# Kernel tuning notes

Measured on AMD Instinct MI355X. Metric: run time of the kernel, lower is better.

Reference implementation:

```python
import jax, jax.numpy as jnp
import numpy as np

D_MODEL = 1024
N_HEADS = 16
D_HEAD = D_MODEL // N_HEADS


def setup_inputs() -> dict:
    key = jax.random.key(0)
    kx, kq, kk, kv, ko = jax.random.split(key, 5)
    s = 1.0 / np.sqrt(D_MODEL)
    return {
        "x": jax.random.normal(kx, (4, 2048, D_MODEL), dtype=jnp.float32),
        "Wq": jax.random.normal(kq, (D_MODEL, D_MODEL), dtype=jnp.float32) * s,
        "Wk": jax.random.normal(kk, (D_MODEL, D_MODEL), dtype=jnp.float32) * s,
        "Wv": jax.random.normal(kv, (D_MODEL, D_MODEL), dtype=jnp.float32) * s,
        "Wo": jax.random.normal(ko, (D_MODEL, D_MODEL), dtype=jnp.float32) * s,
    }


def reference(x, Wq, Wk, Wv, Wo):
    B, L, D = x.shape
    # Projections (torch Linear: y = x @ W.T)
    q = (x @ Wq.T).reshape(B, L, N_HEADS, D_HEAD).transpose(0, 2, 1, 3)  # [B,H,L,dh]
    k = (x @ Wk.T).reshape(B, L, N_HEADS, D_HEAD).transpose(0, 2, 1, 3)
    v = (x @ Wv.T).reshape(B, L, N_HEADS, D_HEAD).transpose(0, 2, 1, 3)
    scale = 1.0 / np.sqrt(D_HEAD).astype(np.float32)
    scores = jnp.einsum('bhqd,bhkd->bhqk', q, k) * scale  # [B,H,L,L]
    causal = jnp.tril(jnp.ones((L, L), dtype=bool))
    scores = jnp.where(causal[None, None], scores, -jnp.inf)
    attn = jax.nn.softmax(scores, axis=-1)
    out = jnp.einsum('bhqk,bhkd->bhqd', attn, v)  # [B,H,L,dh]
    out = out.transpose(0, 2, 1, 3).reshape(B, L, D)
    return out @ Wo.T
```

## Files before the change

kernel.cpp:

```cpp
#include <hip/hip_runtime.h>

typedef short bf16x8 __attribute__((ext_vector_type(8)));
typedef float f32x4 __attribute__((ext_vector_type(4)));
typedef unsigned short u16;

#define MFMA16x16x32(a, b, c) __builtin_amdgcn_mfma_f32_16x16x32_bf16((a), (b), (c), 0, 0, 0)

#define BATCH 4
#define SEQ 2048
#define DMODEL 1024
#define NHEADS 16
#define DHEAD 64
#define MROWS (BATCH * SEQ)

__device__ __forceinline__ u16 f2bf(float f) {
  unsigned u = __builtin_bit_cast(unsigned, f);
  u += 0x7fffu + ((u >> 16) & 1u);
  return (u16)(u >> 16);
}

template <int CTRL>
__device__ __forceinline__ float dppmov(float x) {
  return __builtin_bit_cast(
      float, __builtin_amdgcn_mov_dpp(__builtin_bit_cast(int, x), CTRL, 0xF, 0xF, false));
}
__device__ __forceinline__ float rowmax16(float x) {
  x = fmaxf(x, dppmov<0x128>(x));
  x = fmaxf(x, dppmov<0x124>(x));
  x = fmaxf(x, dppmov<0x122>(x));
  x = fmaxf(x, dppmov<0x121>(x));
  return x;
}
__device__ __forceinline__ float rowsum16(float x) {
  x += dppmov<0x128>(x);
  x += dppmov<0x124>(x);
  x += dppmov<0x122>(x);
  x += dppmov<0x121>(x);
  return x;
}

__global__ void cvt_f32_bf16(const float* __restrict__ src, u16* __restrict__ dst, int n4) {
  int i = blockIdx.x * blockDim.x + threadIdx.x;
  if (i < n4) {
    float4 v = reinterpret_cast<const float4*>(src)[i];
    ushort4 o;
    o.x = f2bf(v.x); o.y = f2bf(v.y); o.z = f2bf(v.z); o.w = f2bf(v.w);
    reinterpret_cast<ushort4*>(dst)[i] = o;
  }
}

template <int MODE>
__global__ __launch_bounds__(256) void gemm_bt(const u16* __restrict__ A,
                                               const u16* __restrict__ Bm,
                                               void* __restrict__ dst) {
  constexpr int K = 1024;
  constexpr int LSTR = 72;
  __shared__ u16 As[128 * LSTR];
  __shared__ u16 Bs[128 * LSTR];
  const int tid = threadIdx.x;
  const int lane = tid & 63;
  const int w = tid >> 6;
  const int wr = w >> 1, wc = w & 1;
  const int quad = lane >> 4, l16 = lane & 15;
  const int row0 = blockIdx.y * 128, col0 = blockIdx.x * 128;

  f32x4 acc[4][4] = {};

  for (int k0 = 0; k0 < K; k0 += 64) {
    __syncthreads();
#pragma unroll
    for (int i = 0; i < 4; i++) {
      int ch = tid + i * 256;
      int r = ch >> 3, cg = (ch & 7) * 8;
      *reinterpret_cast<bf16x8*>(&As[r * LSTR + cg]) =
          *reinterpret_cast<const bf16x8*>(&A[(row0 + r) * K + k0 + cg]);
      *reinterpret_cast<bf16x8*>(&Bs[r * LSTR + cg]) =
          *reinterpret_cast<const bf16x8*>(&Bm[(col0 + r) * K + k0 + cg]);
    }
    __syncthreads();
#pragma unroll
    for (int ks = 0; ks < 2; ks++) {
      bf16x8 af[4], bfr[4];
#pragma unroll
      for (int i = 0; i < 4; i++)
        af[i] = *reinterpret_cast<const bf16x8*>(
            &As[(wr * 64 + i * 16 + l16) * LSTR + ks * 32 + quad * 8]);
#pragma unroll
      for (int j = 0; j < 4; j++)
        bfr[j] = *reinterpret_cast<const bf16x8*>(
            &Bs[(wc * 64 + j * 16 + l16) * LSTR + ks * 32 + quad * 8]);
#pragma unroll
      for (int i = 0; i < 4; i++)
#pragma unroll
        for (int j = 0; j < 4; j++)
          acc[i][j] = MFMA16x16x32(af[i], bfr[j], acc[i][j]);
    }
  }

#pragma unroll
  for (int i = 0; i < 4; i++)
#pragma unroll
    for (int j = 0; j < 4; j++)
#pragma unroll
      for (int r = 0; r < 4; r++) {
        int row = row0 + wr * 64 + i * 16 + quad * 4 + r;
        int col = col0 + wc * 64 + j * 16 + l16;
        float v = acc[i][j][r];
        if constexpr (MODE == 0 || MODE == 3) {
          u16* q = (u16*)dst;
          int bh = ((row >> 11) << 4) | (col >> 6);
          if constexpr (MODE == 3) v *= 0.125f;
          q[(bh * SEQ + (row & 2047)) * DHEAD + (col & 63)] = f2bf(v);
        } else if constexpr (MODE == 1) {
          u16* q = (u16*)dst;
          int bh = ((row >> 11) << 4) | (col >> 6);
          q[(bh * DHEAD + (col & 63)) * SEQ + (row & 2047)] = f2bf(v);
        } else {
          ((float*)dst)[row * DMODEL + col] = v;
        }
      }
}

__global__ __launch_bounds__(256, 3) void attn_kernel(const u16* __restrict__ Q,
                                                      const u16* __restrict__ Kk,
                                                      const u16* __restrict__ Vt,
                                                      u16* __restrict__ Ao) {
  constexpr int STR = 72;
  __shared__ u16 Ks[64 * STR];
  __shared__ u16 Vs[64 * STR];
  __shared__ u16 Plds[4][32 * STR];
  const int tid = threadIdx.x;
  const int lane = tid & 63;
  const int w = tid >> 6;
  const int quad = lane >> 4, l16 = lane & 15;
  const int bh = blockIdx.x & 63;
  const int qt = 15 - (blockIdx.x >> 6);
  const int b = bh >> 4, h = bh & 15;
  const u16* Qh = Q + bh * SEQ * DHEAD;
  const u16* Kh = Kk + bh * SEQ * DHEAD;
  const u16* Vh = Vt + bh * DHEAD * SEQ;
  const int q0w = qt * 128 + w * 32;
  const int nkt = 2 * qt + 2;

  bf16x8 qf[2][2];
#pragma unroll
  for (int rt = 0; rt < 2; rt++)
#pragma unroll
    for (int ks = 0; ks < 2; ks++)
      qf[rt][ks] = *reinterpret_cast<const bf16x8*>(
          &Qh[(q0w + rt * 16 + l16) * DHEAD + ks * 32 + quad * 8]);

  f32x4 o[2][4] = {};
  float m_i[2][4], l_i[2][4];
#pragma unroll
  for (int rt = 0; rt < 2; rt++)
#pragma unroll
    for (int r = 0; r < 4; r++) { m_i[rt][r] = -1e30f; l_i[rt][r] = 0.f; }

  const int srow = tid >> 3;
  const int scol = (tid & 7) * 8;
  bf16x8 kst[2], vst[2];
  auto load_tile = [&](int kb) {
#pragma unroll
    for (int c = 0; c < 2; c++) {
      int r = srow + c * 32;
      kst[c] = *reinterpret_cast<const bf16x8*>(&Kh[(kb + r) * DHEAD + scol]);
      vst[c] = *reinterpret_cast<const bf16x8*>(&Vh[r * SEQ + kb + scol]);
    }
  };
  auto store_tile = [&]() {
#pragma unroll
    for (int c = 0; c < 2; c++) {
      int r = srow + c * 32;
      *reinterpret_cast<bf16x8*>(&Ks[r * STR + scol]) = kst[c];
      *reinterpret_cast<bf16x8*>(&Vs[r * STR + scol]) = vst[c];
    }
  };

  load_tile(0);
  store_tile();
  __syncthreads();

  for (int kt = 0; kt < nkt; kt++) {
    const int kbase = kt * 64;
    const bool have_next = (kt + 1 < nkt);
    if (have_next) load_tile(kbase + 64);

    if (kbase <= q0w + 31) {
      f32x4 s[2][4];
#pragma unroll
      for (int nt = 0; nt < 4; nt++) {
        bf16x8 kf0 = *reinterpret_cast<const bf16x8*>(&Ks[(nt * 16 + l16) * STR + quad * 8]);
        bf16x8 kf1 = *reinterpret_cast<const bf16x8*>(&Ks[(nt * 16 + l16) * STR + 32 + quad * 8]);
#pragma unroll
        for (int rt = 0; rt < 2; rt++) {
          f32x4 z = {0.f, 0.f, 0.f, 0.f};
          z = MFMA16x16x32(qf[rt][0], kf0, z);
          s[rt][nt] = MFMA16x16x32(qf[rt][1], kf1, z);
        }
      }
      if (kbase + 63 > q0w) {
#pragma unroll
        for (int rt = 0; rt < 2; rt++)
#pragma unroll
          for (int nt = 0; nt < 4; nt++)
#pragma unroll
            for (int r = 0; r < 4; r++) {
              int qrow = q0w + rt * 16 + quad * 4 + r;
              int kcol = kbase + nt * 16 + l16;
              if (kcol > qrow) s[rt][nt][r] = -1e30f;
            }
      }
      float alpha[2][4];
#pragma unroll
      for (int rt = 0; rt < 2; rt++)
#pragma unroll
        for (int r = 0; r < 4; r++) {
          float mx = fmaxf(fmaxf(s[rt][0][r], s[rt][1][r]), fmaxf(s[rt][2][r], s[rt][3][r]));
          mx = rowmax16(mx);
          float mnew = fmaxf(m_i[rt][r], mx);
          alpha[rt][r] = __expf(m_i[rt][r] - mnew);
          m_i[rt][r] = mnew;
        }
#pragma unroll
      for (int rt = 0; rt < 2; rt++)
#pragma unroll
        for (int nt = 0; nt < 4; nt++)
#pragma unroll
          for (int r = 0; r < 4; r++)
            s[rt][nt][r] = __expf(s[rt][nt][r] - m_i[rt][r]);
#pragma unroll
      for (int rt = 0; rt < 2; rt++)
#pragma unroll
        for (int r = 0; r < 4; r++) {
          float rs = (s[rt][0][r] + s[rt][1][r]) + (s[rt][2][r] + s[rt][3][r]);
          rs = rowsum16(rs);
          l_i[rt][r] = l_i[rt][r] * alpha[rt][r] + rs;
        }
#pragma unroll
      for (int rt = 0; rt < 2; rt++)
#pragma unroll
        for (int nt = 0; nt < 4; nt++)
#pragma unroll
          for (int r = 0; r < 4; r++) o[rt][nt][r] *= alpha[rt][r];
      u16* Pw = Plds[w];
#pragma unroll
      for (int rt = 0; rt < 2; rt++)
#pragma unroll
        for (int nt = 0; nt < 4; nt++)
#pragma unroll
          for (int r = 0; r < 4; r++)
            Pw[(rt * 16 + quad * 4 + r) * STR + nt * 16 + l16] = f2bf(s[rt][nt][r]);
      asm volatile("s_waitcnt lgkmcnt(0)" ::: "memory");
      bf16x8 pa[2][2];
#pragma unroll
      for (int rt = 0; rt < 2; rt++)
#pragma unroll
        for (int hh = 0; hh < 2; hh++)
          pa[rt][hh] = *reinterpret_cast<const bf16x8*>(
              &Pw[(rt * 16 + l16) * STR + hh * 32 + quad * 8]);
#pragma unroll
      for (int nt2 = 0; nt2 < 4; nt2++) {
        bf16x8 vf0 = *reinterpret_cast<const bf16x8*>(&Vs[(nt2 * 16 + l16) * STR + quad * 8]);
        bf16x8 vf1 = *reinterpret_cast<const bf16x8*>(&Vs[(nt2 * 16 + l16) * STR + 32 + quad * 8]);
#pragma unroll
        for (int rt = 0; rt < 2; rt++) {
          o[rt][nt2] = MFMA16x16x32(pa[rt][0], vf0, o[rt][nt2]);
          o[rt][nt2] = MFMA16x16x32(pa[rt][1], vf1, o[rt][nt2]);
        }
      }
    }

    if (have_next) {
      __syncthreads();
      store_tile();
      __syncthreads();
    }
  }

#pragma unroll
  for (int rt = 0; rt < 2; rt++)
#pragma unroll
    for (int nt2 = 0; nt2 < 4; nt2++)
#pragma unroll
      for (int r = 0; r < 4; r++) {
        int qrow = q0w + rt * 16 + quad * 4 + r;
        float v = o[rt][nt2][r] / l_i[rt][r];
        Ao[(b * SEQ + qrow) * DMODEL + h * DHEAD + nt2 * 16 + l16] = f2bf(v);
      }
}

extern "C" void kernel_launch(void* const* d_in, const int* in_sizes, int n_in,
                              void* d_out, int out_size, void* d_ws, size_t ws_size,
                              hipStream_t stream) {
  const float* x = (const float*)d_in[0];
  const float* Wq = (const float*)d_in[1];
  const float* Wk = (const float*)d_in[2];
  const float* Wv = (const float*)d_in[3];
  const float* Wo = (const float*)d_in[4];
  float* out = (float*)d_out;

  u16* xb  = (u16*)d_ws;
  u16* wqb = xb  + MROWS * DMODEL;
  u16* wkb = wqb + DMODEL * DMODEL;
  u16* wvb = wkb + DMODEL * DMODEL;
  u16* wob = wvb + DMODEL * DMODEL;
  u16* qb  = wob + DMODEL * DMODEL;
  u16* kb  = qb  + MROWS * DMODEL;
  u16* vtb = kb  + MROWS * DMODEL;
  u16* aob = vtb + MROWS * DMODEL;

  {
    int n4 = MROWS * DMODEL / 4;
    cvt_f32_bf16<<<n4 / 256, 256, 0, stream>>>(x, xb, n4);
    int w4 = DMODEL * DMODEL / 4;
    cvt_f32_bf16<<<w4 / 256, 256, 0, stream>>>(Wq, wqb, w4);
    cvt_f32_bf16<<<w4 / 256, 256, 0, stream>>>(Wk, wkb, w4);
    cvt_f32_bf16<<<w4 / 256, 256, 0, stream>>>(Wv, wvb, w4);
    cvt_f32_bf16<<<w4 / 256, 256, 0, stream>>>(Wo, wob, w4);
  }

  dim3 ggrid(DMODEL / 128, MROWS / 128);
  gemm_bt<3><<<ggrid, 256, 0, stream>>>(xb, wqb, (void*)qb);
  gemm_bt<0><<<ggrid, 256, 0, stream>>>(xb, wkb, (void*)kb);
  gemm_bt<1><<<ggrid, 256, 0, stream>>>(xb, wvb, (void*)vtb);

  attn_kernel<<<BATCH * NHEADS * (SEQ / 128), 256, 0, stream>>>(qb, kb, vtb, aob);

  gemm_bt<2><<<ggrid, 256, 0, stream>>>(aob, wob, (void*)out);
}
```

Baseline: 290.1 us.

## Fuse conversions and QKV GEMMs, use direct global-to-LDS loads, exp2 softmax

Merges the five f32-to-bf16 conversion launches into one kernel and the three Q/K/V projection GEMMs into a single launch with a 24-column-tile grid. The GEMM tile loads now use global_load_lds to write straight into unpadded LDS, removing the register round trip. The Q scale now folds in log2(e), so the attention softmax can use exp2f instead of __expf. The unpadded LDS rows may cause bank conflicts on the fragment reads, and the direct-to-LDS load layout has to match the read pattern.

New measurement: 318.4 us. 9.8% more time.

```diff
diff --git a/kernel.cpp b/kernel.cpp
--- a/kernel.cpp
+++ b/kernel.cpp
@@ -13,10 +13,17 @@
 #define DHEAD 64
 #define MROWS (BATCH * SEQ)
 
+#define QSCALE 0.18033688011112443f
+
 __device__ __forceinline__ u16 f2bf(float f) {
   unsigned u = __builtin_bit_cast(unsigned, f);
   u += 0x7fffu + ((u >> 16) & 1u);
   return (u16)(u >> 16);
+}
+
+__device__ __forceinline__ void gl_lds16(const u16* g, u16* l) {
+  __builtin_amdgcn_global_load_lds((__attribute__((address_space(1))) void*)g,
+                                   (__attribute__((address_space(3))) void*)l, 16, 0, 0);
 }
 
 template <int CTRL>
@@ -39,43 +46,45 @@
   return x;
 }
 
-__global__ void cvt_f32_bf16(const float* __restrict__ src, u16* __restrict__ dst, int n4) {
-  int i = blockIdx.x * blockDim.x + threadIdx.x;
-  if (i < n4) {
-    float4 v = reinterpret_cast<const float4*>(src)[i];
-    ushort4 o;
-    o.x = f2bf(v.x); o.y = f2bf(v.y); o.z = f2bf(v.z); o.w = f2bf(v.w);
-    reinterpret_cast<ushort4*>(dst)[i] = o;
+__global__ void cvt_all(const float* __restrict__ x, const float* __restrict__ wq,
+                        const float* __restrict__ wk, const float* __restrict__ wv,
+                        const float* __restrict__ wo, u16* __restrict__ xb,
+                        u16* __restrict__ wqb, u16* __restrict__ wkb, u16* __restrict__ wvb,
+                        u16* __restrict__ wob) {
+  int blk = blockIdx.x;
+  const float* src;
+  u16* dst;
+  long off;
+  if (blk < 8192) {
+    src = x; dst = xb;
+    off = (long)blk * 256 + threadIdx.x;
+  } else {
+    int ws = (blk - 8192) >> 10;
+    int wb = (blk - 8192) & 1023;
+    src = ws == 0 ? wq : ws == 1 ? wk : ws == 2 ? wv : wo;
+    dst = ws == 0 ? wqb : ws == 1 ? wkb : ws == 2 ? wvb : wob;
+    off = (long)wb * 256 + threadIdx.x;
   }
-}
-
-template <int MODE>
-__global__ __launch_bounds__(256) void gemm_bt(const u16* __restrict__ A,
-                                               const u16* __restrict__ Bm,
-                                               void* __restrict__ dst) {
-  constexpr int K = 1024;
-  constexpr int LSTR = 72;
-  __shared__ u16 As[128 * LSTR];
-  __shared__ u16 Bs[128 * LSTR];
-  const int tid = threadIdx.x;
-  const int lane = tid & 63;
-  const int w = tid >> 6;
+  float4 v = reinterpret_cast<const float4*>(src)[off];
+  ushort4 o;
+  o.x = f2bf(v.x); o.y = f2bf(v.y); o.z = f2bf(v.z); o.w = f2bf(v.w);
+  reinterpret_cast<ushort4*>(dst)[off] = o;
+}
+
+__device__ __forceinline__ void gemm_core(const u16* __restrict__ A, const u16* __restrict__ Bm,
+                                          int row0, int bcol0, u16* As, u16* Bs,
+                                          f32x4 (*acc)[4], int tid) {
+  const int lane = tid & 63, w = tid >> 6;
   const int wr = w >> 1, wc = w & 1;
   const int quad = lane >> 4, l16 = lane & 15;
-  const int row0 = blockIdx.y * 128, col0 = blockIdx.x * 128;
-
-  f32x4 acc[4][4] = {};
-
-  for (int k0 = 0; k0 < K; k0 += 64) {
-    __syncthreads();
+  const int lr = lane >> 3, lc = (lane & 7) * 8;
+
+  for (int k0 = 0; k0 < 1024; k0 += 64) {
 #pragma unroll
     for (int i = 0; i < 4; i++) {
-      int ch = tid + i * 256;
-      int r = ch >> 3, cg = (ch & 7) * 8;
-      *reinterpret_cast<bf16x8*>(&As[r * LSTR + cg]) =
-          *reinterpret_cast<const bf16x8*>(&A[(row0 + r) * K + k0 + cg]);
-      *reinterpret_cast<bf16x8*>(&Bs[r * LSTR + cg]) =
-          *reinterpret_cast<const bf16x8*>(&Bm[(col0 + r) * K + k0 + cg]);
+      int rb = i * 32 + w * 8;
+      gl_lds16(&A[(long)(row0 + rb + lr) * 1024 + k0 + lc], &As[rb * 64]);
+      gl_lds16(&Bm[(long)(bcol0 + rb + lr) * 1024 + k0 + lc], &Bs[rb * 64]);
     }
     __syncthreads();
 #pragma unroll
@@ -84,18 +93,76 @@
 #pragma unroll
       for (int i = 0; i < 4; i++)
         af[i] = *reinterpret_cast<const bf16x8*>(
-            &As[(wr * 64 + i * 16 + l16) * LSTR + ks * 32 + quad * 8]);
+            &As[(wr * 64 + i * 16 + l16) * 64 + ks * 32 + quad * 8]);
 #pragma unroll
       for (int j = 0; j < 4; j++)
         bfr[j] = *reinterpret_cast<const bf16x8*>(
-            &Bs[(wc * 64 + j * 16 + l16) * LSTR + ks * 32 + quad * 8]);
+            &Bs[(wc * 64 + j * 16 + l16) * 64 + ks * 32 + quad * 8]);
 #pragma unroll
       for (int i = 0; i < 4; i++)
 #pragma unroll
         for (int j = 0; j < 4; j++)
           acc[i][j] = MFMA16x16x32(af[i], bfr[j], acc[i][j]);
     }
+    __syncthreads();
   }
+}
+
+__global__ __launch_bounds__(256) void gemm_qkv(const u16* __restrict__ xb,
+                                                const u16* __restrict__ wqb,
+                                                const u16* __restrict__ wkb,
+                                                const u16* __restrict__ wvb,
+                                                u16* __restrict__ qb, u16* __restrict__ kb,
+                                                u16* __restrict__ vtb) {
+  __shared__ u16 As[128 * 64];
+  __shared__ u16 Bs[128 * 64];
+  const int tid = threadIdx.x;
+  const int lane = tid & 63, w = tid >> 6;
+  const int wr = w >> 1, wc = w & 1;
+  const int quad = lane >> 4, l16 = lane & 15;
+  const int row0 = blockIdx.y * 128;
+  const int col0 = blockIdx.x * 128;
+  const int widx = col0 >> 10;
+  const int bcol0 = col0 & 1023;
+  const u16* Bm = widx == 0 ? wqb : (widx == 1 ? wkb : wvb);
+
+  f32x4 acc[4][4] = {};
+  gemm_core(xb, Bm, row0, bcol0, As, Bs, acc, tid);
+
+#pragma unroll
+  for (int i = 0; i < 4; i++)
+#pragma unroll
+    for (int j = 0; j < 4; j++)
+#pragma unroll
+      for (int r = 0; r < 4; r++) {
+        int row = row0 + wr * 64 + i * 16 + quad * 4 + r;
+        int col = bcol0 + wc * 64 + j * 16 + l16;
+        float v = acc[i][j][r];
+        int bh = ((row >> 11) << 4) | (col >> 6);
+        if (widx == 0) {
+          qb[(bh * SEQ + (row & 2047)) * DHEAD + (col & 63)] = f2bf(v * QSCALE);
+        } else if (widx == 1) {
+          kb[(bh * SEQ + (row & 2047)) * DHEAD + (col & 63)] = f2bf(v);
+        } else {
+          vtb[(bh * DHEAD + (col & 63)) * SEQ + (row & 2047)] = f2bf(v);
+        }
+      }
+}
+
+__global__ __launch_bounds__(256) void gemm_out(const u16* __restrict__ aob,
+                                                const u16* __restrict__ wob,
+                                                float* __restrict__ out) {
+  __shared__ u16 As[128 * 64];
+  __shared__ u16 Bs[128 * 64];
+  const int tid = threadIdx.x;
+  const int lane = tid & 63, w = tid >> 6;
+  const int wr = w >> 1, wc = w & 1;
+  const int quad = lane >> 4, l16 = lane & 15;
+  const int row0 = blockIdx.y * 128;
+  const int col0 = blockIdx.x * 128;
+
+  f32x4 acc[4][4] = {};
+  gemm_core(aob, wob, row0, col0, As, Bs, acc, tid);
 
 #pragma unroll
   for (int i = 0; i < 4; i++)
@@ -105,19 +172,7 @@
       for (int r = 0; r < 4; r++) {
         int row = row0 + wr * 64 + i * 16 + quad * 4 + r;
         int col = col0 + wc * 64 + j * 16 + l16;
-        float v = acc[i][j][r];
-        if constexpr (MODE == 0 || MODE == 3) {
-          u16* q = (u16*)dst;
-          int bh = ((row >> 11) << 4) | (col >> 6);
-          if constexpr (MODE == 3) v *= 0.125f;
-          q[(bh * SEQ + (row & 2047)) * DHEAD + (col & 63)] = f2bf(v);
-        } else if constexpr (MODE == 1) {
-          u16* q = (u16*)dst;
-          int bh = ((row >> 11) << 4) | (col >> 6);
-          q[(bh * DHEAD + (col & 63)) * SEQ + (row & 2047)] = f2bf(v);
-        } else {
-          ((float*)dst)[row * DMODEL + col] = v;
-        }
+        out[(long)row * DMODEL + col] = acc[i][j][r];
       }
 }
 
@@ -219,7 +274,7 @@
           float mx = fmaxf(fmaxf(s[rt][0][r], s[rt][1][r]), fmaxf(s[rt][2][r], s[rt][3][r]));
           mx = rowmax16(mx);
           float mnew = fmaxf(m_i[rt][r], mx);
-          alpha[rt][r] = __expf(m_i[rt][r] - mnew);
+          alpha[rt][r] = exp2f(m_i[rt][r] - mnew);
           m_i[rt][r] = mnew;
         }
 #pragma unroll
@@ -228,7 +283,7 @@
         for (int nt = 0; nt < 4; nt++)
 #pragma unroll
           for (int r = 0; r < 4; r++)
-            s[rt][nt][r] = __expf(s[rt][nt][r] - m_i[rt][r]);
+            s[rt][nt][r] = exp2f(s[rt][nt][r] - m_i[rt][r]);
 #pragma unroll
       for (int rt = 0; rt < 2; rt++)
 #pragma unroll
@@ -310,22 +365,11 @@
   u16* vtb = kb  + MROWS * DMODEL;
   u16* aob = vtb + MROWS * DMODEL;
 
-  {
-    int n4 = MROWS * DMODEL / 4;
-    cvt_f32_bf16<<<n4 / 256, 256, 0, stream>>>(x, xb, n4);
-    int w4 = DMODEL * DMODEL / 4;
-    cvt_f32_bf16<<<w4 / 256, 256, 0, stream>>>(Wq, wqb, w4);
-    cvt_f32_bf16<<<w4 / 256, 256, 0, stream>>>(Wk, wkb, w4);
-    cvt_f32_bf16<<<w4 / 256, 256, 0, stream>>>(Wv, wvb, w4);
-    cvt_f32_bf16<<<w4 / 256, 256, 0, stream>>>(Wo, wob, w4);
-  }
-
-  dim3 ggrid(DMODEL / 128, MROWS / 128);
-  gemm_bt<3><<<ggrid, 256, 0, stream>>>(xb, wqb, (void*)qb);
-  gemm_bt<0><<<ggrid, 256, 0, stream>>>(xb, wkb, (void*)kb);
-  gemm_bt<1><<<ggrid, 256, 0, stream>>>(xb, wvb, (void*)vtb);
+  cvt_all<<<12288, 256, 0, stream>>>(x, Wq, Wk, Wv, Wo, xb, wqb, wkb, wvb, wob);
+
+  gemm_qkv<<<dim3(24, 64), 256, 0, stream>>>(xb, wqb, wkb, wvb, qb, kb, vtb);
 
   attn_kernel<<<BATCH * NHEADS * (SEQ / 128), 256, 0, stream>>>(qb, kb, vtb, aob);
 
-  gemm_bt<2><<<ggrid, 256, 0, stream>>>(aob, wob, (void*)out);
-}
+  gemm_out<<<dim3(8, 64), 256, 0, stream>>>(aob, wob, out);
+}
```
